# Performance work log

Hardware: AMD Instinct MI355X
Metric: run time of the kernel (lower is better)

The kernel has to match this reference:

```python
import jax, jax.numpy as jnp
import numpy as np
import math
from jax import lax

D = 256      # d_model
H = 8        # heads
DK = D // H  # 32
P = 16       # patch size
IMG = 224
S = (IMG // P) ** 2 + 1  # 197
B = 64
EPS = 1e-5


def _ln(x, g, b):
    m = jnp.mean(x, axis=-1, keepdims=True)
    v = jnp.mean((x - m) ** 2, axis=-1, keepdims=True)
    return (x - m) / jnp.sqrt(v + EPS) * g + b


def _attn(q_in, k_in, v_in, wq, bq, wk, bk, wv, bv, wo, bo, mask):
    # torch Linear: y = x @ W^T + b
    def heads(x, w, b):
        y = x @ w.T + b
        bsz, s, _ = y.shape
        return y.reshape(bsz, s, H, DK).transpose(0, 2, 1, 3)  # [b,h,s,dk]
    q = heads(q_in, wq, bq)
    k = heads(k_in, wk, bk)
    v = heads(v_in, wv, bv)
    att = jnp.einsum('bhqd,bhkd->bhqk', q, k) / math.sqrt(DK)
    if mask is not None:
        att = jnp.where(mask == 0, -jnp.inf, att)
    att = jax.nn.softmax(att, axis=-1)
    o = jnp.einsum('bhqk,bhkd->bhqd', att, v)
    bsz, s, _ = q_in.shape  # output reshape uses q's shape (faithful to source)
    o = o.transpose(0, 2, 1, 3).reshape(bsz, s, D)
    return o @ wo.T + bo


def _patch_embed(img, conv_w, conv_b, cls, pos):
    x = lax.conv_general_dilated(img, conv_w, window_strides=(P, P),
                                 padding='VALID',
                                 dimension_numbers=('NCHW', 'OIHW', 'NCHW'))
    x = x + conv_b[None, :, None, None]
    bsz = img.shape[0]
    x = x.reshape(bsz, D, -1).transpose(0, 2, 1)  # [B,196,D]
    cls_t = jnp.broadcast_to(cls, (bsz, 1, D))
    x = jnp.concatenate([x, cls_t], axis=1)  # cls appended at END (faithful)
    return x + pos


def setup_inputs() -> dict:
    key = jax.random.key(0)
    ks = iter(jax.random.split(key, 64))
    nrm = lambda shape, s=0.02: jax.random.normal(next(ks), shape, jnp.float32) * s
    inp = {
        'enc_out': jax.random.normal(next(ks), (B, 3, IMG, IMG), jnp.float32),
        'dec_in': jax.random.normal(next(ks), (B, S, D), jnp.float32),
        'mask': jnp.ones((1, 1, S, S), jnp.int32),
        'conv_w': nrm((D, 3, P, P)),
        'conv_b': jnp.zeros((D,), jnp.float32),
        'cls': nrm((1, 1, D), 1.0),
        'pos': nrm((1, S, D), 1.0),
        'ff_w1': nrm((4 * D, D)), 'ff_b1': jnp.zeros((4 * D,), jnp.float32),
        'ff_w2': nrm((D, 4 * D)), 'ff_b2': jnp.zeros((D,), jnp.float32),
        'ln1_g': jnp.ones((D,), jnp.float32), 'ln1_b': jnp.zeros((D,), jnp.float32),
        'ln2_g': jnp.ones((D,), jnp.float32), 'ln2_b': jnp.zeros((D,), jnp.float32),
        'ln3_g': jnp.ones((D,), jnp.float32), 'ln3_b': jnp.zeros((D,), jnp.float32),
    }
    for p in ('a1', 'a2'):
        for n in ('wq', 'wk', 'wv', 'wo'):
            inp[f'{p}_{n}'] = nrm((D, D))
            inp[f'{p}_b{n[1]}'] = jnp.zeros((D,), jnp.float32)
    return inp


def reference(enc_out, dec_in, mask, conv_w, conv_b, cls, pos,
              ff_w1, ff_b1, ff_w2, ff_b2,
              ln1_g, ln1_b, ln2_g, ln2_b, ln3_g, ln3_b,
              a1_wq, a1_bq, a1_wk, a1_bk, a1_wv, a1_bv, a1_wo, a1_bo,
              a2_wq, a2_bq, a2_wk, a2_bk, a2_wv, a2_bv, a2_wo, a2_bo):
    e = _patch_embed(enc_out, conv_w, conv_b, cls, pos)  # [B,197,D]
    x = dec_in
    x = _ln(x + _attn(dec_in, dec_in, dec_in,
                      a1_wq, a1_bq, a1_wk, a1_bk, a1_wv, a1_bv, a1_wo, a1_bo,
                      None), ln1_g, ln1_b)
    # faithful: q=k=enc_out, v=dec_in, with mask
    x = _ln(x + _attn(e, e, dec_in,
                      a2_wq, a2_bq, a2_wk, a2_bk, a2_wv, a2_bv, a2_wo, a2_bo,
                      mask), ln2_g, ln2_b)
    ff = jax.nn.relu(x @ ff_w1.T + ff_b1) @ ff_w2.T + ff_b2
    x = _ln(x + ff, ln3_g, ln3_b)
    return x
```

## Files before the change

kernel.cpp:

```cpp
#include <hip/hip_runtime.h>
#include <hip/hip_bf16.h>
#include <math.h>

#define DMODEL 256
#define NH 8
#define DKH 32
#define SEQ 197
#define BATCH 64
#define NPAT 196
#define FFDIM 1024
#define KCONV 768
#define EPSLN 1e-5f
#define MROWS (BATCH * SEQ)
#define SP 224

typedef __attribute__((ext_vector_type(8))) short short8;
typedef __attribute__((ext_vector_type(4))) short short4v;
typedef __attribute__((ext_vector_type(4))) float floatx4;

__device__ inline short f2b(float f) {
  unsigned u = __float_as_uint(f);
  unsigned r = (u + 0x7FFFu + ((u >> 16) & 1u)) >> 16;
  return (short)r;
}
__device__ inline float b2f(short s) {
  return __uint_as_float(((unsigned)(unsigned short)s) << 16);
}

typedef const __attribute__((address_space(1))) unsigned int gu32;
typedef __attribute__((address_space(3))) unsigned int lu32;
__device__ __forceinline__ void gl_lds16(const void* g, void* l) {
  __builtin_amdgcn_global_load_lds((gu32*)g, (lu32*)l, 16, 0, 0);
}

__device__ __forceinline__ void gemm64_body(
    char* smem, int bx, int by,
    const short* __restrict__ A, const short* __restrict__ W,
    const float* __restrict__ bias, const short* __restrict__ resb,
    float* __restrict__ outf, short* __restrict__ outb,
    int N, int K, int relu)
{
  short* Al = (short*)smem;
  short* Bl = (short*)(smem + 16384);
  const int t = threadIdx.x;
  const int wave = t >> 6, lane = t & 63;
  const int wm = (wave & 1) * 32, wn = (wave >> 1) * 32;
  const int ml = lane & 15, quad = lane >> 4;
  const int m7 = ml & 7;
  const int m0 = bx * 64, n0 = by * 64;

  const int rs = t >> 3;
  const int cs = (t & 7) ^ (rs & 7);
  const short* gA0 = A + (size_t)(m0 + rs) * K + cs * 8;
  const short* gA1 = A + (size_t)(m0 + rs + 32) * K + cs * 8;
  const short* gB0 = W + (size_t)(n0 + rs) * K + cs * 8;
  const short* gB1 = W + (size_t)(n0 + rs + 32) * K + cs * 8;

  int offA[2][2], offB[2][2];
#pragma unroll
  for (int kk = 0; kk < 2; kk++)
#pragma unroll
    for (int i = 0; i < 2; i++) {
      int ra = wm + i * 16 + ml;
      offA[kk][i] = ra * 64 + (((kk * 4 + quad) ^ m7) * 8);
      int rb = wn + i * 16 + ml;
      offB[kk][i] = rb * 64 + (((kk * 4 + quad) ^ m7) * 8);
    }

  floatx4 z = {0.f, 0.f, 0.f, 0.f};
  floatx4 acc[2][2] = {{z, z}, {z, z}};

  const int niter = K >> 6;
  gl_lds16(gA0, Al + t * 8);
  gl_lds16(gA1, Al + t * 8 + 2048);
  gl_lds16(gB0, Bl + t * 8);
  gl_lds16(gB1, Bl + t * 8 + 2048);
  for (int k = 0; k < niter; k++) {
    int cur = k & 1;
    if (k + 1 < niter) {
      int nb = (cur ^ 1) * 4096;
      int k0 = (k + 1) << 6;
      gl_lds16(gA0 + k0, Al + nb + t * 8);
      gl_lds16(gA1 + k0, Al + nb + t * 8 + 2048);
      gl_lds16(gB0 + k0, Bl + nb + t * 8);
      gl_lds16(gB1 + k0, Bl + nb + t * 8 + 2048);
      __builtin_amdgcn_s_waitcnt(0x0F74);
    } else {
      __builtin_amdgcn_s_waitcnt(0x0F70);
    }
    __asm__ volatile("s_barrier" ::: "memory");
    const short* Ac = Al + cur * 4096;
    const short* Bc = Bl + cur * 4096;
#pragma unroll
    for (int kk = 0; kk < 2; kk++) {
      short8 a0 = *(const short8*)&Ac[offA[kk][0]];
      short8 a1 = *(const short8*)&Ac[offA[kk][1]];
      short8 b0 = *(const short8*)&Bc[offB[kk][0]];
      short8 b1 = *(const short8*)&Bc[offB[kk][1]];
      acc[0][0] = __builtin_amdgcn_mfma_f32_16x16x32_bf16(a0, b0, acc[0][0], 0, 0, 0);
      acc[0][1] = __builtin_amdgcn_mfma_f32_16x16x32_bf16(a0, b1, acc[0][1], 0, 0, 0);
      acc[1][0] = __builtin_amdgcn_mfma_f32_16x16x32_bf16(a1, b0, acc[1][0], 0, 0, 0);
      acc[1][1] = __builtin_amdgcn_mfma_f32_16x16x32_bf16(a1, b1, acc[1][1], 0, 0, 0);
    }
    __asm__ volatile("s_barrier" ::: "memory");
  }
#pragma unroll
  for (int i = 0; i < 2; i++)
#pragma unroll
    for (int j = 0; j < 2; j++)
#pragma unroll
      for (int rr = 0; rr < 4; rr++) {
        int row = m0 + wm + i * 16 + quad * 4 + rr;
        int col = n0 + wn + j * 16 + ml;
        float v = acc[i][j][rr] + bias[col];
        if (resb) v += b2f(resb[(size_t)row * N + col]);
        if (relu) v = fmaxf(v, 0.f);
        if (outf) outf[(size_t)row * N + col] = v;
        if (outb) outb[(size_t)row * N + col] = f2b(v);
      }
}

__device__ __forceinline__ void gemm_full_body(
    char* smem, int bx,
    const short* __restrict__ A, const short* __restrict__ W,
    const float* __restrict__ bias, const short* __restrict__ resb,
    const float* __restrict__ g, const float* __restrict__ bln,
    short* __restrict__ outb, float* __restrict__ outfin, int K)
{
  short* Al = (short*)smem;
  short* Bl = (short*)(smem + 8192);
  const int t = threadIdx.x;
  const int wave = t >> 6, lane = t & 63;
  const int ml = lane & 15, quad = lane >> 4;
  const int m0 = bx * 64;

  const int rs = t >> 2;
  const int cs = (t & 3) ^ (rs & 3);
  const short* gA = A + (size_t)(m0 + rs) * K + cs * 8;
  const short* gB[4];
#pragma unroll
  for (int j = 0; j < 4; j++)
    gB[j] = W + (size_t)(j * 64 + rs) * K + cs * 8;

  const int offA = (wave * 16 + ml) * 32 + ((quad ^ (ml & 3)) * 8);
  const int offBb = ml * 32 + ((quad ^ (ml & 3)) * 8);

  floatx4 zv = {0.f, 0.f, 0.f, 0.f};
  floatx4 acc[16];
#pragma unroll
  for (int jj = 0; jj < 16; jj++) acc[jj] = zv;

  const int niter = K >> 5;
  gl_lds16(gA, Al + t * 8);
#pragma unroll
  for (int j = 0; j < 4; j++) gl_lds16(gB[j], Bl + j * 2048 + t * 8);
  for (int k = 0; k < niter; k++) {
    int cur = k & 1;
    if (k + 1 < niter) {
      int k0 = (k + 1) << 5;
      int nbA = (cur ^ 1) * 2048, nbB = (cur ^ 1) * 8192;
      gl_lds16(gA + k0, Al + nbA + t * 8);
#pragma unroll
      for (int j = 0; j < 4; j++) gl_lds16(gB[j] + k0, Bl + nbB + j * 2048 + t * 8);
      __builtin_amdgcn_s_waitcnt(0x0F75);
    } else {
      __builtin_amdgcn_s_waitcnt(0x0F70);
    }
    __asm__ volatile("s_barrier" ::: "memory");
    const short* Ac = Al + cur * 2048;
    const short* Bc = Bl + cur * 8192;
    short8 a = *(const short8*)&Ac[offA];
#pragma unroll
    for (int jj = 0; jj < 16; jj++) {
      short8 b = *(const short8*)&Bc[offBb + jj * 512];
      acc[jj] = __builtin_amdgcn_mfma_f32_16x16x32_bf16(a, b, acc[jj], 0, 0, 0);
    }
    __asm__ volatile("s_barrier" ::: "memory");
  }

  const int rbase = m0 + wave * 16 + quad * 4;
  float bias_r[16], g_r[16], bl_r[16];
#pragma unroll
  for (int jj = 0; jj < 16; jj++) {
    int c = jj * 16 + ml;
    bias_r[jj] = bias[c];
    g_r[jj] = g[c];
    bl_r[jj] = bln[c];
  }
#pragma unroll
  for (int jj = 0; jj < 16; jj++)
#pragma unroll
    for (int rr = 0; rr < 4; rr++)
      acc[jj][rr] += bias_r[jj] + b2f(resb[(size_t)(rbase + rr) * DMODEL + jj * 16 + ml]);
#pragma unroll
  for (int rr = 0; rr < 4; rr++) {
    float s = 0.f;
#pragma unroll
    for (int jj = 0; jj < 16; jj++) s += acc[jj][rr];
    s += __shfl_xor(s, 1); s += __shfl_xor(s, 2);
    s += __shfl_xor(s, 4); s += __shfl_xor(s, 8);
    float mean = s * (1.0f / DMODEL);
    float vs = 0.f;
#pragma unroll
    for (int jj = 0; jj < 16; jj++) {
      float d = acc[jj][rr] - mean;
      vs += d * d;
    }
    vs += __shfl_xor(vs, 1); vs += __shfl_xor(vs, 2);
    vs += __shfl_xor(vs, 4); vs += __shfl_xor(vs, 8);
    float inv = rsqrtf(vs * (1.0f / DMODEL) + EPSLN);
    int row = rbase + rr;
#pragma unroll
    for (int jj = 0; jj < 16; jj++) {
      float o = (acc[jj][rr] - mean) * inv * g_r[jj] + bl_r[jj];
      int col = jj * 16 + ml;
      if (outb) outb[(size_t)row * DMODEL + col] = f2b(o);
      if (outfin) outfin[(size_t)row * DMODEL + col] = o;
    }
  }
}

__device__ __forceinline__ void conv64_body(
    char* smem, int bx, int by,
    const float* __restrict__ img, const short* __restrict__ W,
    const float* __restrict__ cb, const float* __restrict__ pos,
    short* __restrict__ e)
{
  short* Al = (short*)smem;
  short* Bl = (short*)(smem + 8192);
  const int t = threadIdx.x;
  const int wave = t >> 6, lane = t & 63;
  const int wm = (wave & 1) * 32, wn = (wave >> 1) * 32;
  const int ml = lane & 15, quad = lane >> 4;
  const int m7 = ml & 7;
  const int m0 = bx * 64, n0 = by * 64;

  int rA = t >> 3, cg = t & 7;
  int pr_off = cg >> 1;
  int px_off = (cg & 1) * 8;
  int csw = cg ^ (rA & 7);
  const float* baseA[2];
  short* lA[2];
#pragma unroll
  for (int p = 0; p < 2; p++) {
    int m = m0 + rA + p * 32;
    int b = m / NPAT, pp = m - b * NPAT;
    int py = pp / 14, px = pp - py * 14;
    baseA[p] = img + (size_t)b * 3 * 50176 + (size_t)(py * 16) * 224 + px * 16 + px_off;
    lA[p] = &Al[(rA + p * 32) * 64 + csw * 8];
  }
  int rs = t >> 3;
  int cs = (t & 7) ^ (rs & 7);
  const short* gB0 = W + (size_t)(n0 + rs) * KCONV + cs * 8;
  const short* gB1 = W + (size_t)(n0 + rs + 32) * KCONV + cs * 8;

  int offA[2][2], offB[2][2];
#pragma unroll
  for (int kk = 0; kk < 2; kk++)
#pragma unroll
    for (int i = 0; i < 2; i++) {
      int ra = wm + i * 16 + ml;
      offA[kk][i] = ra * 64 + (((kk * 4 + quad) ^ m7) * 8);
      int rb = wn + i * 16 + ml;
      offB[kk][i] = rb * 64 + (((kk * 4 + quad) ^ m7) * 8);
    }

  floatx4 z = {0.f, 0.f, 0.f, 0.f};
  floatx4 acc[2][2] = {{z, z}, {z, z}};

  for (int k0 = 0; k0 < KCONV; k0 += 64) {
    int ch = k0 >> 8;
    int rr0 = (k0 & 255) >> 4;
    __syncthreads();
    gl_lds16(gB0 + k0, Bl + t * 8);
    gl_lds16(gB1 + k0, Bl + t * 8 + 2048);
#pragma unroll
    for (int p = 0; p < 2; p++) {
      const float* ap = baseA[p] + (size_t)ch * 50176 + (rr0 + pr_off) * 224;
      float4 a0 = *(const float4*)ap;
      float4 a1 = *(const float4*)(ap + 4);
      short8 av;
      av[0] = f2b(a0.x); av[1] = f2b(a0.y); av[2] = f2b(a0.z); av[3] = f2b(a0.w);
      av[4] = f2b(a1.x); av[5] = f2b(a1.y); av[6] = f2b(a1.z); av[7] = f2b(a1.w);
      *(short8*)lA[p] = av;
    }
    __builtin_amdgcn_s_waitcnt(0x0F70);
    __syncthreads();
#pragma unroll
    for (int kk = 0; kk < 2; kk++) {
      short8 a0 = *(const short8*)&Al[offA[kk][0]];
      short8 a1 = *(const short8*)&Al[offA[kk][1]];
      short8 b0 = *(const short8*)&Bl[offB[kk][0]];
      short8 b1 = *(const short8*)&Bl[offB[kk][1]];
      acc[0][0] = __builtin_amdgcn_mfma_f32_16x16x32_bf16(a0, b0, acc[0][0], 0, 0, 0);
      acc[0][1] = __builtin_amdgcn_mfma_f32_16x16x32_bf16(a0, b1, acc[0][1], 0, 0, 0);
      acc[1][0] = __builtin_amdgcn_mfma_f32_16x16x32_bf16(a1, b0, acc[1][0], 0, 0, 0);
      acc[1][1] = __builtin_amdgcn_mfma_f32_16x16x32_bf16(a1, b1, acc[1][1], 0, 0, 0);
    }
  }
#pragma unroll
  for (int i = 0; i < 2; i++)
#pragma unroll
    for (int j = 0; j < 2; j++)
#pragma unroll
      for (int rr = 0; rr < 4; rr++) {
        int mrow = m0 + wm + i * 16 + quad * 4 + rr;
        int b2 = mrow / NPAT, p2 = mrow - b2 * NPAT;
        int col = n0 + wn + j * 16 + ml;
        e[((size_t)b2 * SEQ + p2) * DMODEL + col] =
            f2b(acc[i][j][rr] + cb[col] + pos[p2 * DMODEL + col]);
      }
}

__device__ __forceinline__ void attn_body(
    char* smem, int bid2,
    const short* __restrict__ qp, int qstr,
    const short* __restrict__ kp, int kstr,
    const short* __restrict__ vp, int vstr,
    const unsigned long long* __restrict__ mbits,
    short* __restrict__ op)
{
  short (*ks)[40] = (short(*)[40])smem;
  short (*vt)[SP + 8] = (short(*)[SP + 8])(smem + 17920);
  short* psw = (short*)(smem + 32768);
  int bh = bid2 >> 1, half = bid2 & 1;
  int b = bh >> 3, h = bh & 7;
  int t = threadIdx.x;
  int wave = t >> 6, lane = t & 63;
  int ml = lane & 15, quad = lane >> 4;
  short* ps = psw + wave * 640;

  const short* kb = kp + (size_t)b * SEQ * kstr + h * DKH;
  const short* vb = vp + (size_t)b * SEQ * vstr + h * DKH;
  for (int idx = t; idx < SEQ * 4; idx += 256) {
    int s = idx >> 2, c = (idx & 3) * 8;
    *(short8*)&ks[s][c] = *(const short8*)(kb + (size_t)s * kstr + c);
  }
  for (int idx = t; idx < SEQ * 4; idx += 256) {
    int s = idx >> 2, c = (idx & 3) * 8;
    short8 v8 = *(const short8*)(vb + (size_t)s * vstr + c);
#pragma unroll
    for (int j = 0; j < 8; j++) vt[c + j][s] = v8[j];
  }
  for (int idx = t; idx < DKH * (SP - SEQ); idx += 256) {
    int d = idx / (SP - SEQ), j = SEQ + idx - d * (SP - SEQ);
    vt[d][j] = 0;
  }
  __syncthreads();

  const float scale = 0.17677669529663687f;
  floatx4 z = {0.f, 0.f, 0.f, 0.f};

  for (int tt = 0; tt < 2; tt++) {
    int ti = half * 8 + wave * 2 + tt;
    int q0 = ti * 16;
    if (q0 >= SEQ) continue;
    int qrow = q0 + ml;
    int qc = qrow < SEQ ? qrow : SEQ - 1;
    short8 qf = *(const short8*)(qp + ((size_t)b * SEQ + qc) * qstr + h * DKH + quad * 8);
    const unsigned long long* mrow = mbits + (size_t)qc * 4;

    floatx4 accO0 = z, accO1 = z;
    float mrun = -1e30f, lrun = 0.f;

    for (int st = 0; st < 7; st++) {
      int j0 = st * 32;
      short8 k0 = *(const short8*)&ks[j0 + ml][quad * 8];
      short8 k1 = *(const short8*)&ks[j0 + 16 + ml][quad * 8];
      floatx4 s0 = __builtin_amdgcn_mfma_f32_16x16x32_bf16(k0, qf, z, 0, 0, 0);
      floatx4 s1 = __builtin_amdgcn_mfma_f32_16x16x32_bf16(k1, qf, z, 0, 0, 0);
      unsigned long long mb = mrow[j0 >> 6] >> (j0 & 63);
      float sv[8];
#pragma unroll
      for (int r = 0; r < 4; r++) {
        int jl = quad * 4 + r;
        sv[r]     = ((mb >> jl) & 1ull)        ? s0[r] * scale : -1e38f;
        sv[4 + r] = ((mb >> (16 + jl)) & 1ull) ? s1[r] * scale : -1e38f;
      }
      float tm = sv[0];
#pragma unroll
      for (int i = 1; i < 8; i++) tm = fmaxf(tm, sv[i]);
      tm = fmaxf(tm, __shfl_xor(tm, 16));
      tm = fmaxf(tm, __shfl_xor(tm, 32));
      float nm = fmaxf(mrun, tm);
      float alpha = __expf(mrun - nm);
      float pv[8];
      float psum = 0.f;
#pragma unroll
      for (int i = 0; i < 8; i++) { pv[i] = __expf(sv[i] - nm); psum += pv[i]; }
      psum += __shfl_xor(psum, 16);
      psum += __shfl_xor(psum, 32);
      lrun = lrun * alpha + psum;
      mrun = nm;
      accO0 = accO0 * alpha;
      accO1 = accO1 * alpha;
      short4v p0, p1;
#pragma unroll
      for (int r = 0; r < 4; r++) { p0[r] = f2b(pv[r]); p1[r] = f2b(pv[4 + r]); }
      *(short4v*)&ps[ml * 40 + quad * 4]      = p0;
      *(short4v*)&ps[ml * 40 + 16 + quad * 4] = p1;
      __asm__ volatile("s_waitcnt lgkmcnt(0)" ::: "memory");
      short8 pf = *(const short8*)&ps[ml * 40 + quad * 8];
      short8 vf0 = *(const short8*)&vt[ml][j0 + quad * 8];
      short8 vf1 = *(const short8*)&vt[16 + ml][j0 + quad * 8];
      accO0 = __builtin_amdgcn_mfma_f32_16x16x32_bf16(vf0, pf, accO0, 0, 0, 0);
      accO1 = __builtin_amdgcn_mfma_f32_16x16x32_bf16(vf1, pf, accO1, 0, 0, 0);
    }
    if (qrow < SEQ) {
      float inv = 1.f / lrun;
      short* ob = op + ((size_t)b * SEQ + qrow) * DMODEL + h * DKH;
      short4v o0, o1;
#pragma unroll
      for (int r = 0; r < 4; r++) {
        o0[r] = f2b(accO0[r] * inv);
        o1[r] = f2b(accO1[r] * inv);
      }
      *(short4v*)(ob + quad * 4)      = o0;
      *(short4v*)(ob + 16 + quad * 4) = o1;
    }
  }
}

__global__ __launch_bounds__(256) void phase0(
    const float* wq1, const float* wk1, const float* wv1,
    const float* bq1, const float* bk1, const float* bv1,
    const float* wq2, const float* wk2, const float* bq2, const float* bk2,
    const float* wv2s, const float* wo1, const float* wo2,
    const float* ffw1, const float* ffw2, const float* convw,
    short* Wqkv1, float* Bqkv1, short* Wqk2, float* Bqk2,
    short* Wv2, short* Wo1, short* Wo2, short* Wff1, short* Wff2, short* Wconv,
    const int* mask, unsigned long long* bits, unsigned long long* ones,
    const float* cls, const float* pos, short* e,
    const float* dec, short* dec_bf)
{
  int bid = blockIdx.x;
  int t = threadIdx.x;
  if (bid < 1024) {
    int i = bid * 256 + t;
    if (i < 65536) {
      Wqkv1[i] = f2b(wq1[i]); Wqkv1[65536 + i] = f2b(wk1[i]); Wqkv1[131072 + i] = f2b(wv1[i]);
      Wqk2[i] = f2b(wq2[i]);  Wqk2[65536 + i] = f2b(wk2[i]);
      Wv2[i] = f2b(wv2s[i]);  Wo1[i] = f2b(wo1[i]);  Wo2[i] = f2b(wo2[i]);
    }
    Wff1[i] = f2b(ffw1[i]); Wff2[i] = f2b(ffw2[i]);
    if (i < 196608) Wconv[i] = f2b(convw[i]);
    if (i < 256) {
      Bqkv1[i] = bq1[i]; Bqkv1[256 + i] = bk1[i]; Bqkv1[512 + i] = bv1[i];
      Bqk2[i] = bq2[i];  Bqk2[256 + i] = bk2[i];
    }
  } else if (bid < 1028) {
    int idx = (bid - 1024) * 256 + t;
    if (idx < SEQ * 4) {
      int r = idx >> 2, w = idx & 3;
      unsigned long long bb = 0ull, oo = 0ull;
      for (int j = 0; j < 64; j++) {
        int c = w * 64 + j;
        if (c < SEQ) {
          oo |= (1ull << j);
          if (mask[r * SEQ + c] != 0) bb |= (1ull << j);
        }
      }
      bits[idx] = bb;
      ones[idx] = oo;
    }
  } else if (bid < 1092) {
    int b = bid - 1028, d = t;
    e[((size_t)b * SEQ + NPAT) * DMODEL + d] = f2b(cls[d] + pos[NPAT * DMODEL + d]);
  } else {
    const int ND = (MROWS * DMODEL) / 8;
    int i = (bid - 1092) * 256 + t;
    if (i < ND) {
      float4 a0 = ((const float4*)dec)[i * 2];
      float4 a1 = ((const float4*)dec)[i * 2 + 1];
      short8 o;
      o[0] = f2b(a0.x); o[1] = f2b(a0.y); o[2] = f2b(a0.z); o[3] = f2b(a0.w);
      o[4] = f2b(a1.x); o[5] = f2b(a1.y); o[6] = f2b(a1.z); o[7] = f2b(a1.w);
      ((short8*)dec_bf)[i] = o;
    }
  }
}

__global__ __launch_bounds__(256) void phase1(
    const float* __restrict__ enc, const short* __restrict__ Wconv,
    const float* __restrict__ conv_b, const float* __restrict__ pos,
    short* __restrict__ e_bf,
    const short* __restrict__ dec_bf,
    const short* __restrict__ Wqkv1, const float* __restrict__ Bqkv1,
    short* __restrict__ qkv1,
    const short* __restrict__ Wv2, const float* __restrict__ bv2,
    short* __restrict__ v2)
{
  __shared__ char smem[32768];
  int bid = blockIdx.x;
  if (bid < 784) {
    conv64_body(smem, bid >> 2, bid & 3, enc, Wconv, conv_b, pos, e_bf);
  } else if (bid < 3148) {
    int idx = bid - 784;
    gemm64_body(smem, idx / 12, idx % 12, dec_bf, Wqkv1, Bqkv1, nullptr,
                nullptr, qkv1, 768, 256, 0);
  } else {
    int idx = bid - 3148;
    gemm64_body(smem, idx >> 2, idx & 3, dec_bf, Wv2, bv2, nullptr,
                nullptr, v2, 256, 256, 0);
  }
}

__global__ __launch_bounds__(256) void phase2(
    const short* __restrict__ qkv1, const unsigned long long* __restrict__ mones,
    short* __restrict__ o1,
    const short* __restrict__ e_bf, const short* __restrict__ Wqk2,
    const float* __restrict__ Bqk2, short* __restrict__ qk2)
{
  __shared__ char smem[37888];
  int bid = blockIdx.x;
  if (bid < 1024) {
    attn_body(smem, bid, qkv1, 768, qkv1 + 256, 768, qkv1 + 512, 768, mones, o1);
  } else {
    int idx = bid - 1024;
    gemm64_body(smem, idx >> 3, idx & 7, e_bf, Wqk2, Bqk2, nullptr,
                nullptr, qk2, 512, 256, 0);
  }
}

__global__ __launch_bounds__(256) void phase3(
    const short* __restrict__ qk2, const short* __restrict__ v2,
    const unsigned long long* __restrict__ mbits, short* __restrict__ o2,
    const short* __restrict__ o1, const short* __restrict__ Wo1,
    const float* __restrict__ bo1, const short* __restrict__ dec_bf,
    const float* __restrict__ ln1_g, const float* __restrict__ ln1_b,
    short* __restrict__ x1b)
{
  __shared__ char smem[40960];
  int bid = blockIdx.x;
  if (bid < 1024) {
    attn_body(smem, bid, qk2, 512, qk2 + 256, 512, v2, 256, mbits, o2);
  } else {
    gemm_full_body(smem, bid - 1024, o1, Wo1, bo1, dec_bf, ln1_g, ln1_b,
                   x1b, nullptr, 256);
  }
}

__global__ __launch_bounds__(256) void gemm_full_k(
    const short* __restrict__ A, const short* __restrict__ W,
    const float* __restrict__ bias, const short* __restrict__ resb,
    const float* __restrict__ g, const float* __restrict__ bln,
    short* __restrict__ outb, float* __restrict__ outfin, int K)
{
  __shared__ char smem[40960];
  gemm_full_body(smem, blockIdx.x, A, W, bias, resb, g, bln, outb, outfin, K);
}

__global__ __launch_bounds__(256) void gemm_k(
    const short* __restrict__ A, const short* __restrict__ W,
    const float* __restrict__ bias, const short* __restrict__ resb,
    float* __restrict__ outf, short* __restrict__ outb,
    int N, int K, int relu, int nby)
{
  __shared__ char smem[32768];
  gemm64_body(smem, blockIdx.x / nby, blockIdx.x % nby, A, W, bias, resb,
              outf, outb, N, K, relu);
}

extern "C" void kernel_launch(void* const* d_in, const int* in_sizes, int n_in,
                              void* d_out, int out_size, void* d_ws, size_t ws_size,
                              hipStream_t stream)
{
  const float* enc    = (const float*)d_in[0];
  const float* dec_in = (const float*)d_in[1];
  const int*   mask   = (const int*)  d_in[2];
  const float* conv_w = (const float*)d_in[3];
  const float* conv_b = (const float*)d_in[4];
  const float* cls    = (const float*)d_in[5];
  const float* pos    = (const float*)d_in[6];
  const float* ff_w1  = (const float*)d_in[7];
  const float* ff_b1  = (const float*)d_in[8];
  const float* ff_w2  = (const float*)d_in[9];
  const float* ff_b2  = (const float*)d_in[10];
  const float* ln1_g  = (const float*)d_in[11];
  const float* ln1_b  = (const float*)d_in[12];
  const float* ln2_g  = (const float*)d_in[13];
  const float* ln2_b  = (const float*)d_in[14];
  const float* ln3_g  = (const float*)d_in[15];
  const float* ln3_b  = (const float*)d_in[16];
  const float* a1_wq = (const float*)d_in[17]; const float* a1_bq = (const float*)d_in[18];
  const float* a1_wk = (const float*)d_in[19]; const float* a1_bk = (const float*)d_in[20];
  const float* a1_wv = (const float*)d_in[21]; const float* a1_bv = (const float*)d_in[22];
  const float* a1_wo = (const float*)d_in[23]; const float* a1_bo = (const float*)d_in[24];
  const float* a2_wq = (const float*)d_in[25]; const float* a2_bq = (const float*)d_in[26];
  const float* a2_wk = (const float*)d_in[27]; const float* a2_bk = (const float*)d_in[28];
  const float* a2_wv = (const float*)d_in[29]; const float* a2_bv = (const float*)d_in[30];
  const float* a2_wo = (const float*)d_in[31]; const float* a2_bo = (const float*)d_in[32];

  char* wsB = (char*)d_ws;
  short* Wqkv1 = (short*)wsB;
  short* Wqk2  = Wqkv1 + 196608;
  short* Wv2   = Wqk2 + 131072;
  short* Wo1   = Wv2 + 65536;
  short* Wo2   = Wo1 + 65536;
  short* Wff1  = Wo2 + 65536;
  short* Wff2  = Wff1 + 262144;
  short* Wconv = Wff2 + 262144;
  float* Bqkv1 = (float*)(Wconv + 196608);
  float* Bqk2  = Bqkv1 + 768;
  unsigned long long* mbits = (unsigned long long*)(Bqk2 + 512);
  unsigned long long* mones = mbits + 788;

  const size_t MB = 1048576;
  short* dec_bf = (short*)(wsB + 3 * MB);
  short* e_bf   = (short*)(wsB + 10 * MB);
  short* qkv1   = (short*)(wsB + 17 * MB);
  short* o1     = (short*)(wsB + 37 * MB);
  short* qk2    = (short*)(wsB + 44 * MB);
  short* v2     = (short*)(wsB + 57 * MB);
  short* h_buf  = (short*)(wsB + 64 * MB);
  short* x1b    = (short*)(wsB + 97 * MB);
  short* x2b    = (short*)(wsB + 104 * MB);
  short* o2     = o1;

  dim3 blk(256);

  phase0<<<2668, blk, 0, stream>>>(
      a1_wq, a1_wk, a1_wv, a1_bq, a1_bk, a1_bv,
      a2_wq, a2_wk, a2_bq, a2_bk, a2_wv, a1_wo, a2_wo,
      ff_w1, ff_w2, conv_w,
      Wqkv1, Bqkv1, Wqk2, Bqk2, Wv2, Wo1, Wo2, Wff1, Wff2, Wconv,
      mask, mbits, mones, cls, pos, e_bf, dec_in, dec_bf);

  phase1<<<3936, blk, 0, stream>>>(
      enc, Wconv, conv_b, pos, e_bf,
      dec_bf, Wqkv1, Bqkv1, qkv1, Wv2, a2_bv, v2);

  phase2<<<2600, blk, 0, stream>>>(
      qkv1, mones, o1, e_bf, Wqk2, Bqk2, qk2);

  phase3<<<1221, blk, 0, stream>>>(
      qk2, v2, mbits, o2, o1, Wo1, a1_bo, dec_bf, ln1_g, ln1_b, x1b);

  gemm_full_k<<<197, blk, 0, stream>>>(
      o2, Wo2, a2_bo, x1b, ln2_g, ln2_b, x2b, nullptr, 256);

  gemm_k<<<3152, blk, 0, stream>>>(
      x2b, Wff1, ff_b1, nullptr, nullptr, h_buf, FFDIM, 256, 1, 16);

  gemm_full_k<<<197, blk, 0, stream>>>(
      h_buf, Wff2, ff_b2, x2b, ln3_g, ln3_b, nullptr, (float*)d_out, 1024);
}
```

Baseline: 338.8 us.

## Give each attention block a full head and split fused phase3 into two kernels

Each attention block now handles one (batch, head) pair and all 13 query tiles across its 4 waves, instead of two blocks per head that each reload the same K/V into LDS. The V transpose load is reordered so consecutive lanes write consecutive sequence positions, which is meant to cut LDS bank conflicts. The LDS swizzle in the full-row GEMM now XORs in higher row bits to spread bank accesses. The fused phase3 becomes a separate Wo1+LN GEMM launch followed by the cross-attention launch. That ordering also removes a hazard where o2 aliases o1 while both were read and written in one launch, at the cost of an extra launch and less overlap.

New measurement: 326.8 us. 3.5% less time.

```diff
diff --git a/kernel.cpp b/kernel.cpp
--- a/kernel.cpp
+++ b/kernel.cpp
@@ -135,15 +135,16 @@
   const int m0 = bx * 64;
 
   const int rs = t >> 2;
-  const int cs = (t & 3) ^ (rs & 3);
+  const int cs = (t & 3) ^ ((rs ^ (rs >> 2)) & 3);
   const short* gA = A + (size_t)(m0 + rs) * K + cs * 8;
   const short* gB[4];
 #pragma unroll
   for (int j = 0; j < 4; j++)
     gB[j] = W + (size_t)(j * 64 + rs) * K + cs * 8;
 
-  const int offA = (wave * 16 + ml) * 32 + ((quad ^ (ml & 3)) * 8);
-  const int offBb = ml * 32 + ((quad ^ (ml & 3)) * 8);
+  const int sm = (ml ^ (ml >> 2)) & 3;
+  const int offA = (wave * 16 + ml) * 32 + ((quad ^ sm) * 8);
+  const int offBb = ml * 32 + ((quad ^ sm) * 8);
 
   floatx4 zv = {0.f, 0.f, 0.f, 0.f};
   floatx4 acc[16];
@@ -313,7 +314,7 @@
 }
 
 __device__ __forceinline__ void attn_body(
-    char* smem, int bid2,
+    char* smem, int bh,
     const short* __restrict__ qp, int qstr,
     const short* __restrict__ kp, int kstr,
     const short* __restrict__ vp, int vstr,
@@ -323,7 +324,6 @@
   short (*ks)[40] = (short(*)[40])smem;
   short (*vt)[SP + 8] = (short(*)[SP + 8])(smem + 17920);
   short* psw = (short*)(smem + 32768);
-  int bh = bid2 >> 1, half = bid2 & 1;
   int b = bh >> 3, h = bh & 7;
   int t = threadIdx.x;
   int wave = t >> 6, lane = t & 63;
@@ -336,11 +336,14 @@
     int s = idx >> 2, c = (idx & 3) * 8;
     *(short8*)&ks[s][c] = *(const short8*)(kb + (size_t)s * kstr + c);
   }
-  for (int idx = t; idx < SEQ * 4; idx += 256) {
-    int s = idx >> 2, c = (idx & 3) * 8;
-    short8 v8 = *(const short8*)(vb + (size_t)s * vstr + c);
-#pragma unroll
-    for (int j = 0; j < 8; j++) vt[c + j][s] = v8[j];
+  for (int idx = t; idx < 1024; idx += 256) {
+    int s = ((idx >> 8) << 6) + (idx & 63);
+    int c = ((idx >> 6) & 3) * 8;
+    if (s < SEQ) {
+      short8 v8 = *(const short8*)(vb + (size_t)s * vstr + c);
+#pragma unroll
+      for (int j = 0; j < 8; j++) vt[c + j][s] = v8[j];
+    }
   }
   for (int idx = t; idx < DKH * (SP - SEQ); idx += 256) {
     int d = idx / (SP - SEQ), j = SEQ + idx - d * (SP - SEQ);
@@ -351,10 +354,8 @@
   const float scale = 0.17677669529663687f;
   floatx4 z = {0.f, 0.f, 0.f, 0.f};
 
-  for (int tt = 0; tt < 2; tt++) {
-    int ti = half * 8 + wave * 2 + tt;
+  for (int ti = wave; ti < 13; ti += 4) {
     int q0 = ti * 16;
-    if (q0 >= SEQ) continue;
     int qrow = q0 + ml;
     int qc = qrow < SEQ ? qrow : SEQ - 1;
     short8 qf = *(const short8*)(qp + ((size_t)b * SEQ + qc) * qstr + h * DKH + quad * 8);
@@ -513,31 +514,24 @@
 {
   __shared__ char smem[37888];
   int bid = blockIdx.x;
-  if (bid < 1024) {
+  if (bid < 512) {
     attn_body(smem, bid, qkv1, 768, qkv1 + 256, 768, qkv1 + 512, 768, mones, o1);
   } else {
-    int idx = bid - 1024;
+    int idx = bid - 512;
     gemm64_body(smem, idx >> 3, idx & 7, e_bf, Wqk2, Bqk2, nullptr,
                 nullptr, qk2, 512, 256, 0);
   }
 }
 
-__global__ __launch_bounds__(256) void phase3(
-    const short* __restrict__ qk2, const short* __restrict__ v2,
-    const unsigned long long* __restrict__ mbits, short* __restrict__ o2,
-    const short* __restrict__ o1, const short* __restrict__ Wo1,
-    const float* __restrict__ bo1, const short* __restrict__ dec_bf,
-    const float* __restrict__ ln1_g, const float* __restrict__ ln1_b,
-    short* __restrict__ x1b)
-{
-  __shared__ char smem[40960];
-  int bid = blockIdx.x;
-  if (bid < 1024) {
-    attn_body(smem, bid, qk2, 512, qk2 + 256, 512, v2, 256, mbits, o2);
-  } else {
-    gemm_full_body(smem, bid - 1024, o1, Wo1, bo1, dec_bf, ln1_g, ln1_b,
-                   x1b, nullptr, 256);
-  }
+__global__ __launch_bounds__(256) void attn_k(
+    const short* __restrict__ qp, int qstr,
+    const short* __restrict__ kp, int kstr,
+    const short* __restrict__ vp, int vstr,
+    const unsigned long long* __restrict__ mbits,
+    short* __restrict__ op)
+{
+  __shared__ char smem[37888];
+  attn_body(smem, blockIdx.x, qp, qstr, kp, kstr, vp, vstr, mbits, op);
 }
 
 __global__ __launch_bounds__(256) void gemm_full_k(
@@ -630,11 +624,14 @@
       enc, Wconv, conv_b, pos, e_bf,
       dec_bf, Wqkv1, Bqkv1, qkv1, Wv2, a2_bv, v2);
 
-  phase2<<<2600, blk, 0, stream>>>(
+  phase2<<<2088, blk, 0, stream>>>(
       qkv1, mones, o1, e_bf, Wqk2, Bqk2, qk2);
 
-  phase3<<<1221, blk, 0, stream>>>(
-      qk2, v2, mbits, o2, o1, Wo1, a1_bo, dec_bf, ln1_g, ln1_b, x1b);
+  gemm_full_k<<<197, blk, 0, stream>>>(
+      o1, Wo1, a1_bo, dec_bf, ln1_g, ln1_b, x1b, nullptr, 256);
+
+  attn_k<<<512, blk, 0, stream>>>(
+      qk2, 512, qk2 + 256, 512, v2, 256, mbits, o2);
 
   gemm_full_k<<<197, blk, 0, stream>>>(
       o2, Wo2, a2_bo, x1b, ln2_g, ln2_b, x2b, nullptr, 256);
```
